# Kernel optimization log

Hardware: AMD Instinct MI355X
Metric: run time of the kernel (lower is better)

## Reference

```python
import jax, jax.numpy as jnp
import numpy as np

N_HEADS = 16

def setup_inputs() -> dict:
    key = jax.random.key(0)
    k1, k2, k3 = jax.random.split(key, 3)
    d = 1024
    x = jax.random.normal(k1, (2, 2048, d), dtype=jnp.float32)
    W_in = jax.random.normal(k2, (d, 3 * d), dtype=jnp.float32) * (d ** -0.5)
    W_out = jax.random.normal(k3, (d, d), dtype=jnp.float32) * (d ** -0.5)
    return {"x": x, "W_in": W_in, "W_out": W_out}

def reference(x, W_in, W_out):
    B, S, D = x.shape
    H = N_HEADS
    Dh = D // H
    qkv = x @ W_in                                  # [B,S,3D]
    q, k, v = jnp.split(qkv, 3, axis=-1)
    # [B,S,D] -> [B,H,S,Dh]
    q = q.reshape(B, S, H, Dh).transpose(0, 2, 1, 3)
    k = k.reshape(B, S, H, Dh).transpose(0, 2, 1, 3)
    v = v.reshape(B, S, H, Dh).transpose(0, 2, 1, 3)
    scores = jnp.einsum('bhqd,bhkd->bhqk', q, k)    # [B,H,S,S]
    causal = jnp.triu(jnp.ones((S, S), dtype=bool), k=1)
    scores = jnp.where(causal, -jnp.inf, scores)
    scores = scores / jnp.sqrt(jnp.asarray(Dh, scores.dtype))
    attn = jax.nn.softmax(scores, axis=-1)
    out = jnp.einsum('bhqk,bhkd->bhqd', attn, v)    # [B,H,S,Dh]
    out = out.transpose(0, 2, 1, 3).reshape(B, S, D)
    return out @ W_out
```

## Files before the change

kernel.cpp:

```cpp
#include <hip/hip_runtime.h>
#include <cstdint>
#include <cstddef>

typedef __bf16 bf16;
typedef bf16  bf16x4  __attribute__((ext_vector_type(4)));
typedef bf16  bf16x8  __attribute__((ext_vector_type(8)));
typedef float floatx4 __attribute__((ext_vector_type(4)));

#define BATCH 2
#define SEQ   2048
#define DIM   1024
#define NH    16
#define DH    64
#define D3    3072
#define MROWS 4096

__device__ __forceinline__ void gld16(void* lds, const void* gptr) {
  __builtin_amdgcn_global_load_lds(
      (const __attribute__((address_space(1))) unsigned int*)gptr,
      (__attribute__((address_space(3))) unsigned int*)lds, 16, 0, 0);
}

__global__ __launch_bounds__(256) void k_prep(const float4* __restrict__ x,
                                              bf16* __restrict__ xb,
                                              const float* __restrict__ Wi,
                                              bf16* __restrict__ wti,
                                              const float* __restrict__ Wo,
                                              bf16* __restrict__ wto) {
  __shared__ float tile[32][33];
  const int bid = blockIdx.x;
  if (bid < 4096) {
    int i = bid * 256 + threadIdx.x;
    float4 v = x[i];
    bf16x4 o;
    o.x = (bf16)v.x; o.y = (bf16)v.y; o.z = (bf16)v.z; o.w = (bf16)v.w;
    *(bf16x4*)(xb + (size_t)i * 4) = o;
    return;
  }
  const float* W; bf16* Wt; int N, id;
  if (bid < 7168) { W = Wi; Wt = wti; N = 3072; id = bid - 4096; }
  else            { W = Wo; Wt = wto; N = 1024; id = bid - 7168; }
  const int nb = N / 32;
  int n0 = (id % nb) * 32, k0 = (id / nb) * 32;
  int tx = threadIdx.x & 31, ty = threadIdx.x >> 5;
#pragma unroll
  for (int i = 0; i < 4; i++)
    tile[ty + i * 8][tx] = W[(size_t)(k0 + ty + i * 8) * N + n0 + tx];
  __syncthreads();
#pragma unroll
  for (int i = 0; i < 4; i++)
    Wt[(size_t)(n0 + ty + i * 8) * 1024 + k0 + tx] = (bf16)tile[tx][ty + i * 8];
}

__global__ __launch_bounds__(256, 2) void k_gemm1(const bf16* __restrict__ A,
                                                  const bf16* __restrict__ Bt,
                                                  bf16* __restrict__ qk,
                                                  bf16* __restrict__ vt) {
  constexpr int K = DIM;
  constexpr int nk = K / 64;
  __shared__ __align__(16) bf16 As[2][128 * 64];
  __shared__ __align__(16) bf16 Bs[2][192 * 64];

  const int t = threadIdx.x, l = t & 63, w = t >> 6;
  const int q = l >> 4, mm = l & 15;
  const int wm = w >> 1, wn = w & 1;

  const int xcd = blockIdx.x & 7, j = blockIdx.x >> 3;
  const int by = ((xcd >> 1) << 3) + (j >> 3);
  const int bx = ((xcd & 1) << 3) + (j & 7);
  const int m0 = by * 128, n0 = bx * 192;

  auto stA = [&](int T, int up) {
    const int bp = T & 1;
#pragma unroll
    for (int i = 0; i < 2; i++) {
      int c = t + i * 256;
      int rl = c >> 3, pos = c & 7;
      int row = ((rl >> 5) << 6) + (up << 5) + (rl & 31);
      int gs = pos ^ (row & 7);
      gld16((char*)(As[bp] + row * 64 + pos * 8),
            A + (size_t)(m0 + row) * K + T * 64 + gs * 8);
    }
  };
  auto stB = [&](int T, int up) {
    const int bp = T & 1;
#pragma unroll
    for (int i = 0; i < 3; i++) {
      int c = t + i * 256;
      int rl = c >> 3, pos = c & 7;
      int row = up * 96 + rl;
      int gs = pos ^ (row & 7);
      gld16((char*)(Bs[bp] + row * 64 + pos * 8),
            Bt + (size_t)(n0 + row) * K + T * 64 + gs * 8);
    }
  };

  floatx4 acc[4][6] = {};

  stA(0, 0); stB(0, 0); stA(0, 1); stB(0, 1);
  stA(1, 0); stB(1, 0);

  for (int T = 0; T < nk; T++) {
    const int bp = T & 1;
    if (T + 1 < nk)
      asm volatile("s_waitcnt vmcnt(5)\n\ts_barrier" ::: "memory");
    else
      asm volatile("s_waitcnt vmcnt(0)\n\ts_barrier" ::: "memory");

    const bf16* Ab = As[bp] + wm * 64 * 64;
    const bf16* Bb = Bs[bp] + wn * 96 * 64;
    bf16x8 a0[2][2], a1[2][2], b0[3][2], b1[3][2];

#pragma unroll
    for (int mt = 0; mt < 2; mt++)
#pragma unroll
      for (int kk = 0; kk < 2; kk++)
        a0[mt][kk] = *(const bf16x8*)(Ab + (size_t)(mt * 16 + mm) * 64 +
                                      ((kk * 4 + q) ^ (mm & 7)) * 8);
#pragma unroll
    for (int nt = 0; nt < 3; nt++)
#pragma unroll
      for (int kk = 0; kk < 2; kk++)
        b0[nt][kk] = *(const bf16x8*)(Bb + (size_t)(nt * 16 + mm) * 64 +
                                      ((kk * 4 + q) ^ (mm & 7)) * 8);
    if (T + 1 < nk) stA(T + 1, 1);
    asm volatile("s_barrier" ::: "memory");
    __builtin_amdgcn_s_setprio(1);
#pragma unroll
    for (int mt = 0; mt < 2; mt++)
#pragma unroll
      for (int nt = 0; nt < 3; nt++)
#pragma unroll
        for (int kk = 0; kk < 2; kk++)
          acc[mt][nt] = __builtin_amdgcn_mfma_f32_16x16x32_bf16(
              a0[mt][kk], b0[nt][kk], acc[mt][nt], 0, 0, 0);
    __builtin_amdgcn_s_setprio(0);
    asm volatile("s_barrier" ::: "memory");

#pragma unroll
    for (int nt = 0; nt < 3; nt++)
#pragma unroll
      for (int kk = 0; kk < 2; kk++)
        b1[nt][kk] = *(const bf16x8*)(Bb + (size_t)((3 + nt) * 16 + mm) * 64 +
                                      ((kk * 4 + q) ^ (mm & 7)) * 8);
    if (T + 1 < nk) stB(T + 1, 1);
    asm volatile("s_barrier" ::: "memory");
    __builtin_amdgcn_s_setprio(1);
#pragma unroll
    for (int mt = 0; mt < 2; mt++)
#pragma unroll
      for (int nt = 0; nt < 3; nt++)
#pragma unroll
        for (int kk = 0; kk < 2; kk++)
          acc[mt][3 + nt] = __builtin_amdgcn_mfma_f32_16x16x32_bf16(
              a0[mt][kk], b1[nt][kk], acc[mt][3 + nt], 0, 0, 0);
    __builtin_amdgcn_s_setprio(0);
    asm volatile("s_barrier" ::: "memory");

#pragma unroll
    for (int mt = 0; mt < 2; mt++)
#pragma unroll
      for (int kk = 0; kk < 2; kk++)
        a1[mt][kk] = *(const bf16x8*)(Ab + (size_t)(32 + mt * 16 + mm) * 64 +
                                      ((kk * 4 + q) ^ (mm & 7)) * 8);
    if (T + 2 < nk) stA(T + 2, 0);
    asm volatile("s_barrier" ::: "memory");
    __builtin_amdgcn_s_setprio(1);
#pragma unroll
    for (int mt = 0; mt < 2; mt++)
#pragma unroll
      for (int nt = 0; nt < 3; nt++)
#pragma unroll
        for (int kk = 0; kk < 2; kk++)
          acc[2 + mt][nt] = __builtin_amdgcn_mfma_f32_16x16x32_bf16(
              a1[mt][kk], b0[nt][kk], acc[2 + mt][nt], 0, 0, 0);
    __builtin_amdgcn_s_setprio(0);
    asm volatile("s_barrier" ::: "memory");

    if (T + 2 < nk) stB(T + 2, 0);
    asm volatile("s_barrier" ::: "memory");
    __builtin_amdgcn_s_setprio(1);
#pragma unroll
    for (int mt = 0; mt < 2; mt++)
#pragma unroll
      for (int nt = 0; nt < 3; nt++)
#pragma unroll
        for (int kk = 0; kk < 2; kk++)
          acc[2 + mt][3 + nt] = __builtin_amdgcn_mfma_f32_16x16x32_bf16(
              a1[mt][kk], b1[nt][kk], acc[2 + mt][3 + nt], 0, 0, 0);
    __builtin_amdgcn_s_setprio(0);
  }

#pragma unroll
  for (int mt = 0; mt < 4; mt++)
#pragma unroll
    for (int nt = 0; nt < 6; nt++) {
      int row = m0 + wm * 64 + mt * 16 + q * 4;
      int col = n0 + wn * 96 + nt * 16 + mm;
      if (col < 2048) {
#pragma unroll
        for (int r = 0; r < 4; r++)
          qk[(size_t)(row + r) * 2048 + col] = (bf16)acc[mt][nt][r];
      } else {
        int d = col - 2048;
        int hh = d >> 6, dh = d & 63;
#pragma unroll
        for (int r = 0; r < 4; r++) {
          int rr = row + r;
          int bb = rr >> 11, s = rr & 2047;
          vt[((size_t)(bb * 16 + hh) * 64 + dh) * SEQ + s] = (bf16)acc[mt][nt][r];
        }
      }
    }
}

template <typename OutT, int MODE, int BN>
__global__ __launch_bounds__(256) void k_gemm_bt(const bf16* __restrict__ A,
                                                 const bf16* __restrict__ Bt,
                                                 OutT* __restrict__ C,
                                                 bf16* __restrict__ qk,
                                                 bf16* __restrict__ vt,
                                                 int M, int N, int K) {
  constexpr int LN = 2 + BN / 64;
  __shared__ __align__(16) bf16 As[3][128 * 32];
  __shared__ __align__(16) bf16 Bs[3][BN * 32];
  const int t = threadIdx.x, l = t & 63, w = t >> 6;
  const int q = l >> 4, mm = l & 15;
  const int m0 = blockIdx.y * 128, n0 = blockIdx.x * BN;
  constexpr int MT = (BN == 128) ? 4 : 2;
  const int mo = (BN == 128) ? ((w >> 1) * 64) : (w * 32);
  const int no = (BN == 128) ? ((w & 1) * 64) : 0;
  const int sw = (mm >> 1) & 3;

  auto stage = [&](int kt) {
    const int bp = kt % 3;
#pragma unroll
    for (int i = 0; i < 2; i++) {
      int c = t + i * 256;
      int row = c >> 2, pos = c & 3;
      int gs = pos ^ ((row >> 1) & 3);
      gld16((char*)As[bp] + (size_t)c * 16, A + (size_t)(m0 + row) * K + kt * 32 + gs * 8);
    }
#pragma unroll
    for (int i = 0; i < BN / 64; i++) {
      int c = t + i * 256;
      int row = c >> 2, pos = c & 3;
      int gs = pos ^ ((row >> 1) & 3);
      gld16((char*)Bs[bp] + (size_t)c * 16, Bt + (size_t)(n0 + row) * K + kt * 32 + gs * 8);
    }
  };

  floatx4 acc[MT][4] = {};
  const int nk = K >> 5;

  stage(0);
  stage(1);

  for (int kt = 0; kt < nk; kt++) {
    if (kt + 1 < nk)
      asm volatile("s_waitcnt vmcnt(%0)\n\ts_barrier" :: "n"(LN) : "memory");
    else
      asm volatile("s_waitcnt vmcnt(0)\n\ts_barrier" ::: "memory");
    if (kt + 2 < nk) stage(kt + 2);

    const bf16* Ab = As[kt % 3];
    const bf16* Bb = Bs[kt % 3];
    bf16x8 af[MT], bfr[4];
#pragma unroll
    for (int mt = 0; mt < MT; mt++)
      af[mt] = *(const bf16x8*)(Ab + (size_t)(mo + mt * 16 + mm) * 32 + (q ^ sw) * 8);
#pragma unroll
    for (int nt = 0; nt < 4; nt++)
      bfr[nt] = *(const bf16x8*)(Bb + (size_t)(no + nt * 16 + mm) * 32 + (q ^ sw) * 8);
#pragma unroll
    for (int mt = 0; mt < MT; mt++)
#pragma unroll
      for (int nt = 0; nt < 4; nt++)
        acc[mt][nt] = __builtin_amdgcn_mfma_f32_16x16x32_bf16(af[mt], bfr[nt],
                                                              acc[mt][nt], 0, 0, 0);
  }
#pragma unroll
  for (int mt = 0; mt < MT; mt++)
#pragma unroll
    for (int nt = 0; nt < 4; nt++)
#pragma unroll
      for (int r = 0; r < 4; r++) {
        int row = m0 + mo + mt * 16 + q * 4 + r;
        int col = n0 + no + nt * 16 + mm;
        if (MODE == 0) {
          C[(size_t)row * N + col] = (OutT)acc[mt][nt][r];
        } else {
          if (col < 2048) {
            qk[(size_t)row * 2048 + col] = (bf16)acc[mt][nt][r];
          } else {
            int d = col - 2048;
            int hh = d >> 6, dh = d & 63;
            int bb = row >> 11, s = row & 2047;
            vt[((size_t)(bb * 16 + hh) * 64 + dh) * SEQ + s] = (bf16)acc[mt][nt][r];
          }
        }
      }
}

__global__ __launch_bounds__(256, 4) void k_attn(const bf16* __restrict__ qk,
                                                 const bf16* __restrict__ vt,
                                                 bf16* __restrict__ out) {
  const int bx = blockIdx.x;
  const int qt = 31 - (bx >> 5);
  const int bh = bx & 31;
  const int b = bh >> 4, h = bh & 15;
  const int t = threadIdx.x, l = t & 63, w = t >> 6;
  const int q4 = l >> 4, mm = l & 15;
  const int sw = (mm >> 1) & 3;

  __shared__ __align__(16) char lds[8192 + 16384 + 16384];
  bf16* Qs = (bf16*)lds;
  bf16* Ps = (bf16*)lds;
  bf16* Ks = (bf16*)(lds + 8192);
  bf16* Vs = (bf16*)(lds + 8192 + 16384);

  const size_t qkbase = (size_t)b * SEQ * 2048;
  const size_t vtbase = (size_t)bh * 64 * SEQ;

  auto stage = [&](int kt) {
    const int bp = kt & 1;
#pragma unroll
    for (int i = 0; i < 2; i++) {
      int row = t >> 2, pos = t & 3;
      int g = pos ^ ((row >> 1) & 3);
      gld16((char*)(Ks + bp * 4096) + ((size_t)t + i * 256) * 16,
            qk + qkbase + (size_t)(kt * 64 + row) * 2048 + 1024 + h * 64 + i * 32 + g * 8);
    }
#pragma unroll
    for (int i = 0; i < 2; i++) {
      int c = t + i * 256;
      int vr = c >> 3, vc = c & 7;
      int src = vc ^ (vr & 7);
      gld16((char*)(Vs + bp * 4096) + (size_t)c * 16,
            vt + vtbase + (size_t)vr * SEQ + kt * 64 + src * 8);
    }
  };

  {
    int row = t >> 2, col = (t & 3) * 8;
#pragma unroll
    for (int i = 0; i < 2; i++)
      gld16((char*)Qs + ((size_t)t + i * 256) * 16,
            qk + qkbase + (size_t)(qt * 64 + row) * 2048 + h * 64 + i * 32 + col);
  }
  stage(0);
  __syncthreads();
  bf16x8 qf[2];
#pragma unroll
  for (int ks = 0; ks < 2; ks++) {
    qf[ks] = *(const bf16x8*)(Qs + (size_t)(ks * 64 + w * 16 + mm) * 32 + q4 * 8);
#pragma unroll
    for (int j = 0; j < 8; j++)
      qf[ks][j] = (bf16)((float)qf[ks][j] * 0.18033688f);
  }
  __syncthreads();

  float l_i = 0.f;
  floatx4 oaccT[4] = {};
  const int qloc = w * 16 + mm;
  const float FM = 24.0f;

  bf16* Pw = Ps + (size_t)w * 640;

  for (int kt = 0; kt <= qt; kt++) {
    if (kt < qt) stage(kt + 1);
    const bf16* Kb = Ks + (kt & 1) * 4096;
    const bf16* Vb = Vs + (kt & 1) * 4096;

    floatx4 sacc[4] = {};
#pragma unroll
    for (int ks = 0; ks < 2; ks++)
#pragma unroll
      for (int ct = 0; ct < 4; ct++) {
        bf16x8 kf = *(const bf16x8*)(Kb + (size_t)(ks * 64 + ct * 16 + mm) * 32 + (q4 ^ sw) * 8);
        sacc[ct] = __builtin_amdgcn_mfma_f32_16x16x32_bf16(kf, qf[ks], sacc[ct], 0, 0, 0);
      }

    bf16x4 pk[4];
    float rsum = 0.f;
    if (kt == qt) {
#pragma unroll
      for (int ct = 0; ct < 4; ct++)
#pragma unroll
        for (int r = 0; r < 4; r++) {
          float e = (ct * 16 + q4 * 4 + r > qloc)
                        ? 0.f : __builtin_amdgcn_exp2f(sacc[ct][r] - FM);
          pk[ct][r] = (bf16)e;
          rsum += e;
        }
    } else {
#pragma unroll
      for (int ct = 0; ct < 4; ct++)
#pragma unroll
        for (int r = 0; r < 4; r++) {
          float e = __builtin_amdgcn_exp2f(sacc[ct][r] - FM);
          pk[ct][r] = (bf16)e;
          rsum += e;
        }
    }
    rsum += __shfl_xor(rsum, 16, 64);
    rsum += __shfl_xor(rsum, 32, 64);
    l_i += rsum;

#pragma unroll
    for (int ks = 0; ks < 2; ks++) {
      *(bf16x4*)(Pw + (size_t)mm * 40 + q4 * 4)      = pk[ks * 2 + 0];
      *(bf16x4*)(Pw + (size_t)mm * 40 + 16 + q4 * 4) = pk[ks * 2 + 1];
      bf16x8 pf = *(const bf16x8*)(Pw + (size_t)mm * 40 + q4 * 8);
#pragma unroll
      for (int nt = 0; nt < 4; nt++) {
        int chunk = (ks * 4 + q4) ^ (mm & 7);
        bf16x8 vf = *(const bf16x8*)(Vb + (size_t)(nt * 16 + mm) * 64 + chunk * 8);
        oaccT[nt] = __builtin_amdgcn_mfma_f32_16x16x32_bf16(vf, pf, oaccT[nt], 0, 0, 0);
      }
    }

    if (kt < qt) __syncthreads();
  }

  float inv = 1.0f / l_i;
  int qrow = qt * 64 + qloc;
  bf16* orow = out + ((size_t)b * SEQ + qrow) * DIM + h * 64;
#pragma unroll
  for (int nt = 0; nt < 4; nt++) {
    bf16x4 o4;
#pragma unroll
    for (int r = 0; r < 4; r++) o4[r] = (bf16)(oaccT[nt][r] * inv);
    *(bf16x4*)(orow + nt * 16 + q4 * 4) = o4;
  }
}

extern "C" void kernel_launch(void* const* d_in, const int* in_sizes, int n_in,
                              void* d_out, int out_size, void* d_ws, size_t ws_size,
                              hipStream_t stream) {
  const float* x     = (const float*)d_in[0];
  const float* W_in  = (const float*)d_in[1];
  const float* W_out = (const float*)d_in[2];
  float* out = (float*)d_out;

  char* ws = (char*)d_ws;
  bf16* xb   = (bf16*)(ws);
  bf16* wti  = (bf16*)(ws + 8388608);
  bf16* wto  = (bf16*)(ws + 14680064);
  bf16* qkb  = (bf16*)(ws + 16777216);
  bf16* vtb  = (bf16*)(ws + 33554432);
  bf16* attn = xb;

  k_prep<<<8192, 256, 0, stream>>>((const float4*)x, xb, W_in, wti, W_out, wto);
  k_gemm1<<<512, 256, 0, stream>>>(xb, wti, qkb, vtb);
  k_attn<<<1024, 256, 0, stream>>>(qkb, vtb, attn);
  k_gemm_bt<float, 0, 64><<<dim3(16, 32), 256, 0, stream>>>(attn, wto, out, nullptr, nullptr,
                                                            MROWS, DIM, DIM);
}
```

Before: 163.3 us.

## Double attention query tile to 128 rows per block to reuse K/V tiles

Each attention block now handles 128 query rows instead of 64: every wave holds two 16-row query groups and issues two MFMAs per K/V fragment load, which halves the K/V global-to-LDS traffic per query. The grid shrinks from 1024 to 512 blocks, LDS grows to 48KB and launch bounds drop to 2 blocks per CU to allow more registers. The cost is lower occupancy, fewer blocks for load balancing under the causal triangle, and extra masked work on the two diagonal tiles.

New measurement: 170.7 us. 4.6% more time.

```diff
diff --git a/kernel.cpp b/kernel.cpp
--- a/kernel.cpp
+++ b/kernel.cpp
@@ -302,22 +302,22 @@
       }
 }
 
-__global__ __launch_bounds__(256, 4) void k_attn(const bf16* __restrict__ qk,
+__global__ __launch_bounds__(256, 2) void k_attn(const bf16* __restrict__ qk,
                                                  const bf16* __restrict__ vt,
                                                  bf16* __restrict__ out) {
   const int bx = blockIdx.x;
-  const int qt = 31 - (bx >> 5);
+  const int qt = 15 - (bx >> 5);
   const int bh = bx & 31;
   const int b = bh >> 4, h = bh & 15;
   const int t = threadIdx.x, l = t & 63, w = t >> 6;
   const int q4 = l >> 4, mm = l & 15;
   const int sw = (mm >> 1) & 3;
 
-  __shared__ __align__(16) char lds[8192 + 16384 + 16384];
+  __shared__ __align__(16) char lds[16384 + 16384 + 16384];
   bf16* Qs = (bf16*)lds;
   bf16* Ps = (bf16*)lds;
-  bf16* Ks = (bf16*)(lds + 8192);
-  bf16* Vs = (bf16*)(lds + 8192 + 16384);
+  bf16* Ks = (bf16*)(lds + 16384);
+  bf16* Vs = (bf16*)(lds + 32768);
 
   const size_t qkbase = (size_t)b * SEQ * 2048;
   const size_t vtbase = (size_t)bh * 64 * SEQ;
@@ -342,96 +342,116 @@
   };
 
   {
-    int row = t >> 2, col = (t & 3) * 8;
-#pragma unroll
-    for (int i = 0; i < 2; i++)
-      gld16((char*)Qs + ((size_t)t + i * 256) * 16,
-            qk + qkbase + (size_t)(qt * 64 + row) * 2048 + h * 64 + i * 32 + col);
+    int row = t >> 2, c8 = (t & 3) * 8;
+#pragma unroll
+    for (int u = 0; u < 2; u++)
+#pragma unroll
+      for (int ks = 0; ks < 2; ks++)
+        gld16((char*)Qs + (size_t)ks * 8192 + u * 4096 + (size_t)t * 16,
+              qk + qkbase + (size_t)(qt * 128 + u * 64 + row) * 2048 + h * 64 + ks * 32 + c8);
   }
   stage(0);
   __syncthreads();
-  bf16x8 qf[2];
-#pragma unroll
-  for (int ks = 0; ks < 2; ks++) {
-    qf[ks] = *(const bf16x8*)(Qs + (size_t)(ks * 64 + w * 16 + mm) * 32 + q4 * 8);
-#pragma unroll
-    for (int j = 0; j < 8; j++)
-      qf[ks][j] = (bf16)((float)qf[ks][j] * 0.18033688f);
-  }
+  bf16x8 qf[2][2];
+#pragma unroll
+  for (int g = 0; g < 2; g++)
+#pragma unroll
+    for (int ks = 0; ks < 2; ks++) {
+      qf[g][ks] = *(const bf16x8*)(Qs + (size_t)ks * 4096 +
+                                   (size_t)(w * 32 + g * 16 + mm) * 32 + q4 * 8);
+#pragma unroll
+      for (int j = 0; j < 8; j++)
+        qf[g][ks][j] = (bf16)((float)qf[g][ks][j] * 0.18033688f);
+    }
   __syncthreads();
 
-  float l_i = 0.f;
-  floatx4 oaccT[4] = {};
-  const int qloc = w * 16 + mm;
+  float l_i[2] = {0.f, 0.f};
+  floatx4 oaccT[2][4] = {};
   const float FM = 24.0f;
-
-  bf16* Pw = Ps + (size_t)w * 640;
-
-  for (int kt = 0; kt <= qt; kt++) {
-    if (kt < qt) stage(kt + 1);
+  const int nkt = 2 * qt + 2;
+
+  bf16* Pw0 = Ps + (size_t)(w * 2 + 0) * 640;
+  bf16* Pw1 = Ps + (size_t)(w * 2 + 1) * 640;
+
+  for (int kt = 0; kt < nkt; kt++) {
+    if (kt + 1 < nkt) stage(kt + 1);
     const bf16* Kb = Ks + (kt & 1) * 4096;
     const bf16* Vb = Vs + (kt & 1) * 4096;
 
-    floatx4 sacc[4] = {};
+    floatx4 sacc[2][4] = {};
 #pragma unroll
     for (int ks = 0; ks < 2; ks++)
 #pragma unroll
       for (int ct = 0; ct < 4; ct++) {
         bf16x8 kf = *(const bf16x8*)(Kb + (size_t)(ks * 64 + ct * 16 + mm) * 32 + (q4 ^ sw) * 8);
-        sacc[ct] = __builtin_amdgcn_mfma_f32_16x16x32_bf16(kf, qf[ks], sacc[ct], 0, 0, 0);
+        sacc[0][ct] = __builtin_amdgcn_mfma_f32_16x16x32_bf16(kf, qf[0][ks], sacc[0][ct], 0, 0, 0);
+        sacc[1][ct] = __builtin_amdgcn_mfma_f32_16x16x32_bf16(kf, qf[1][ks], sacc[1][ct], 0, 0, 0);
       }
 
-    bf16x4 pk[4];
-    float rsum = 0.f;
-    if (kt == qt) {
+    bf16x4 pk[2][4];
+    float rs0 = 0.f, rs1 = 0.f;
+    if (kt >= 2 * qt) {
+      const int kvb = (kt - 2 * qt) * 64;
 #pragma unroll
       for (int ct = 0; ct < 4; ct++)
 #pragma unroll
         for (int r = 0; r < 4; r++) {
-          float e = (ct * 16 + q4 * 4 + r > qloc)
-                        ? 0.f : __builtin_amdgcn_exp2f(sacc[ct][r] - FM);
-          pk[ct][r] = (bf16)e;
-          rsum += e;
+          int kv = kvb + ct * 16 + q4 * 4 + r;
+          float e0 = (kv > w * 32 + mm)      ? 0.f : __builtin_amdgcn_exp2f(sacc[0][ct][r] - FM);
+          float e1 = (kv > w * 32 + 16 + mm) ? 0.f : __builtin_amdgcn_exp2f(sacc[1][ct][r] - FM);
+          pk[0][ct][r] = (bf16)e0; rs0 += e0;
+          pk[1][ct][r] = (bf16)e1; rs1 += e1;
         }
     } else {
 #pragma unroll
       for (int ct = 0; ct < 4; ct++)
 #pragma unroll
         for (int r = 0; r < 4; r++) {
-          float e = __builtin_amdgcn_exp2f(sacc[ct][r] - FM);
-          pk[ct][r] = (bf16)e;
-          rsum += e;
+          float e0 = __builtin_amdgcn_exp2f(sacc[0][ct][r] - FM);
+          float e1 = __builtin_amdgcn_exp2f(sacc[1][ct][r] - FM);
+          pk[0][ct][r] = (bf16)e0; rs0 += e0;
+          pk[1][ct][r] = (bf16)e1; rs1 += e1;
         }
     }
-    rsum += __shfl_xor(rsum, 16, 64);
-    rsum += __shfl_xor(rsum, 32, 64);
-    l_i += rsum;
+    rs0 += __shfl_xor(rs0, 16, 64);
+    rs0 += __shfl_xor(rs0, 32, 64);
+    rs1 += __shfl_xor(rs1, 16, 64);
+    rs1 += __shfl_xor(rs1, 32, 64);
+    l_i[0] += rs0;
+    l_i[1] += rs1;
 
 #pragma unroll
     for (int ks = 0; ks < 2; ks++) {
-      *(bf16x4*)(Pw + (size_t)mm * 40 + q4 * 4)      = pk[ks * 2 + 0];
-      *(bf16x4*)(Pw + (size_t)mm * 40 + 16 + q4 * 4) = pk[ks * 2 + 1];
-      bf16x8 pf = *(const bf16x8*)(Pw + (size_t)mm * 40 + q4 * 8);
+      *(bf16x4*)(Pw0 + (size_t)mm * 40 + q4 * 4)      = pk[0][ks * 2 + 0];
+      *(bf16x4*)(Pw0 + (size_t)mm * 40 + 16 + q4 * 4) = pk[0][ks * 2 + 1];
+      *(bf16x4*)(Pw1 + (size_t)mm * 40 + q4 * 4)      = pk[1][ks * 2 + 0];
+      *(bf16x4*)(Pw1 + (size_t)mm * 40 + 16 + q4 * 4) = pk[1][ks * 2 + 1];
+      bf16x8 pf0 = *(const bf16x8*)(Pw0 + (size_t)mm * 40 + q4 * 8);
+      bf16x8 pf1 = *(const bf16x8*)(Pw1 + (size_t)mm * 40 + q4 * 8);
 #pragma unroll
       for (int nt = 0; nt < 4; nt++) {
         int chunk = (ks * 4 + q4) ^ (mm & 7);
         bf16x8 vf = *(const bf16x8*)(Vb + (size_t)(nt * 16 + mm) * 64 + chunk * 8);
-        oaccT[nt] = __builtin_amdgcn_mfma_f32_16x16x32_bf16(vf, pf, oaccT[nt], 0, 0, 0);
+        oaccT[0][nt] = __builtin_amdgcn_mfma_f32_16x16x32_bf16(vf, pf0, oaccT[0][nt], 0, 0, 0);
+        oaccT[1][nt] = __builtin_amdgcn_mfma_f32_16x16x32_bf16(vf, pf1, oaccT[1][nt], 0, 0, 0);
       }
     }
 
-    if (kt < qt) __syncthreads();
-  }
-
-  float inv = 1.0f / l_i;
-  int qrow = qt * 64 + qloc;
-  bf16* orow = out + ((size_t)b * SEQ + qrow) * DIM + h * 64;
-#pragma unroll
-  for (int nt = 0; nt < 4; nt++) {
-    bf16x4 o4;
-#pragma unroll
-    for (int r = 0; r < 4; r++) o4[r] = (bf16)(oaccT[nt][r] * inv);
-    *(bf16x4*)(orow + nt * 16 + q4 * 4) = o4;
+    if (kt + 1 < nkt) __syncthreads();
+  }
+
+#pragma unroll
+  for (int g = 0; g < 2; g++) {
+    float inv = 1.0f / l_i[g];
+    int qrow = qt * 128 + w * 32 + g * 16 + mm;
+    bf16* orow = out + ((size_t)b * SEQ + qrow) * DIM + h * 64;
+#pragma unroll
+    for (int nt = 0; nt < 4; nt++) {
+      bf16x4 o4;
+#pragma unroll
+      for (int r = 0; r < 4; r++) o4[r] = (bf16)(oaccT[g][nt][r] * inv);
+      *(bf16x4*)(orow + nt * 16 + q4 * 4) = o4;
+    }
   }
 }
 
@@ -453,7 +473,7 @@
 
   k_prep<<<8192, 256, 0, stream>>>((const float4*)x, xb, W_in, wti, W_out, wto);
   k_gemm1<<<512, 256, 0, stream>>>(xb, wti, qkb, vtb);
-  k_attn<<<1024, 256, 0, stream>>>(qkb, vtb, attn);
+  k_attn<<<512, 256, 0, stream>>>(qkb, vtb, attn);
   k_gemm_bt<float, 0, 64><<<dim3(16, 32), 256, 0, stream>>>(attn, wto, out, nullptr, nullptr,
                                                             MROWS, DIM, DIM);
 }
```

## Rewrite output projection GEMM with 64-wide K tiles, split-phase pipelining and XCD-aware mapping

Applied to the files above, without the earlier changes.

Replaces the generic templated GEMM used for the output projection with a dedicated kernel. It uses 64-element K tiles with an 8-way XOR swizzle, a 2x2 warp layout, and A/B global-to-LDS prefetches split across two MFMA phases with s_setprio raised around the MFMAs. It also remaps the 1D block index so that neighbouring tiles land on the same XCD for L2 reuse. The aim is to cut the number of barrier iterations and to overlap loads with compute better. The cost is more LDS per block and extra barriers in each iteration.

Result: faster. 156.6 us (-4.1%).

```diff
diff --git a/kernel.cpp b/kernel.cpp
--- a/kernel.cpp
+++ b/kernel.cpp
@@ -214,92 +214,119 @@
     }
 }
 
-template <typename OutT, int MODE, int BN>
-__global__ __launch_bounds__(256) void k_gemm_bt(const bf16* __restrict__ A,
-                                                 const bf16* __restrict__ Bt,
-                                                 OutT* __restrict__ C,
-                                                 bf16* __restrict__ qk,
-                                                 bf16* __restrict__ vt,
-                                                 int M, int N, int K) {
-  constexpr int LN = 2 + BN / 64;
-  __shared__ __align__(16) bf16 As[3][128 * 32];
-  __shared__ __align__(16) bf16 Bs[3][BN * 32];
+__global__ __launch_bounds__(256, 2) void k_gemm2(const bf16* __restrict__ A,
+                                                  const bf16* __restrict__ Bt,
+                                                  float* __restrict__ C) {
+  constexpr int K = DIM;
+  constexpr int nk = K / 64;
+  constexpr int N = DIM;
+  __shared__ __align__(16) bf16 As[3][128 * 64];
+  __shared__ __align__(16) bf16 Bs[3][64 * 64];
+
   const int t = threadIdx.x, l = t & 63, w = t >> 6;
   const int q = l >> 4, mm = l & 15;
-  const int m0 = blockIdx.y * 128, n0 = blockIdx.x * BN;
-  constexpr int MT = (BN == 128) ? 4 : 2;
-  const int mo = (BN == 128) ? ((w >> 1) * 64) : (w * 32);
-  const int no = (BN == 128) ? ((w & 1) * 64) : 0;
-  const int sw = (mm >> 1) & 3;
-
-  auto stage = [&](int kt) {
-    const int bp = kt % 3;
+  const int wm = w >> 1, wn = w & 1;
+
+  const int xcd = blockIdx.x & 7, j = blockIdx.x >> 3;
+  const int by = ((xcd >> 1) << 3) + (j >> 3);
+  const int bx = ((xcd & 1) << 3) + (j & 7);
+  const int m0 = by * 128, n0 = bx * 64;
+
+  auto stA2 = [&](int T) {
+    const int bp = T % 3;
+#pragma unroll
+    for (int i = 0; i < 4; i++) {
+      int c = t + i * 256;
+      int row = c >> 3, pos = c & 7;
+      int gs = pos ^ (row & 7);
+      gld16((char*)(As[bp] + row * 64 + pos * 8),
+            A + (size_t)(m0 + row) * K + T * 64 + gs * 8);
+    }
+  };
+  auto stB2 = [&](int T) {
+    const int bp = T % 3;
 #pragma unroll
     for (int i = 0; i < 2; i++) {
       int c = t + i * 256;
-      int row = c >> 2, pos = c & 3;
-      int gs = pos ^ ((row >> 1) & 3);
-      gld16((char*)As[bp] + (size_t)c * 16, A + (size_t)(m0 + row) * K + kt * 32 + gs * 8);
-    }
-#pragma unroll
-    for (int i = 0; i < BN / 64; i++) {
-      int c = t + i * 256;
-      int row = c >> 2, pos = c & 3;
-      int gs = pos ^ ((row >> 1) & 3);
-      gld16((char*)Bs[bp] + (size_t)c * 16, Bt + (size_t)(n0 + row) * K + kt * 32 + gs * 8);
+      int row = c >> 3, pos = c & 7;
+      int gs = pos ^ (row & 7);
+      gld16((char*)(Bs[bp] + row * 64 + pos * 8),
+            Bt + (size_t)(n0 + row) * K + T * 64 + gs * 8);
     }
   };
 
-  floatx4 acc[MT][4] = {};
-  const int nk = K >> 5;
-
-  stage(0);
-  stage(1);
-
-  for (int kt = 0; kt < nk; kt++) {
-    if (kt + 1 < nk)
-      asm volatile("s_waitcnt vmcnt(%0)\n\ts_barrier" :: "n"(LN) : "memory");
+  floatx4 acc[4][2] = {};
+
+  stA2(0); stB2(0);
+  stA2(1); stB2(1);
+
+  for (int T = 0; T < nk; T++) {
+    const int bp = T % 3;
+    if (T + 1 < nk)
+      asm volatile("s_waitcnt vmcnt(6)\n\ts_barrier" ::: "memory");
     else
       asm volatile("s_waitcnt vmcnt(0)\n\ts_barrier" ::: "memory");
-    if (kt + 2 < nk) stage(kt + 2);
-
-    const bf16* Ab = As[kt % 3];
-    const bf16* Bb = Bs[kt % 3];
-    bf16x8 af[MT], bfr[4];
-#pragma unroll
-    for (int mt = 0; mt < MT; mt++)
-      af[mt] = *(const bf16x8*)(Ab + (size_t)(mo + mt * 16 + mm) * 32 + (q ^ sw) * 8);
-#pragma unroll
-    for (int nt = 0; nt < 4; nt++)
-      bfr[nt] = *(const bf16x8*)(Bb + (size_t)(no + nt * 16 + mm) * 32 + (q ^ sw) * 8);
-#pragma unroll
-    for (int mt = 0; mt < MT; mt++)
-#pragma unroll
-      for (int nt = 0; nt < 4; nt++)
-        acc[mt][nt] = __builtin_amdgcn_mfma_f32_16x16x32_bf16(af[mt], bfr[nt],
-                                                              acc[mt][nt], 0, 0, 0);
-  }
-#pragma unroll
-  for (int mt = 0; mt < MT; mt++)
-#pragma unroll
-    for (int nt = 0; nt < 4; nt++)
-#pragma unroll
-      for (int r = 0; r < 4; r++) {
-        int row = m0 + mo + mt * 16 + q * 4 + r;
-        int col = n0 + no + nt * 16 + mm;
-        if (MODE == 0) {
-          C[(size_t)row * N + col] = (OutT)acc[mt][nt][r];
-        } else {
-          if (col < 2048) {
-            qk[(size_t)row * 2048 + col] = (bf16)acc[mt][nt][r];
-          } else {
-            int d = col - 2048;
-            int hh = d >> 6, dh = d & 63;
-            int bb = row >> 11, s = row & 2047;
-            vt[((size_t)(bb * 16 + hh) * 64 + dh) * SEQ + s] = (bf16)acc[mt][nt][r];
-          }
-        }
-      }
+
+    const bf16* Ab = As[bp] + wm * 64 * 64;
+    const bf16* Bb = Bs[bp] + wn * 32 * 64;
+    bf16x8 af[4][2], bf[2][2];
+
+#pragma unroll
+    for (int mt = 0; mt < 2; mt++)
+#pragma unroll
+      for (int kk = 0; kk < 2; kk++)
+        af[mt][kk] = *(const bf16x8*)(Ab + (size_t)(mt * 16 + mm) * 64 +
+                                      ((kk * 4 + q) ^ (mm & 7)) * 8);
+#pragma unroll
+    for (int nt = 0; nt < 2; nt++)
+#pragma unroll
+      for (int kk = 0; kk < 2; kk++)
+        bf[nt][kk] = *(const bf16x8*)(Bb + (size_t)(nt * 16 + mm) * 64 +
+                                      ((kk * 4 + q) ^ (mm & 7)) * 8);
+    if (T + 2 < nk) stA2(T + 2);
+    asm volatile("s_barrier" ::: "memory");
+    __builtin_amdgcn_s_setprio(1);
+#pragma unroll
+    for (int mt = 0; mt < 2; mt++)
+#pragma unroll
+      for (int nt = 0; nt < 2; nt++)
+#pragma unroll
+        for (int kk = 0; kk < 2; kk++)
+          acc[mt][nt] = __builtin_amdgcn_mfma_f32_16x16x32_bf16(
+              af[mt][kk], bf[nt][kk], acc[mt][nt], 0, 0, 0);
+    __builtin_amdgcn_s_setprio(0);
+    asm volatile("s_barrier" ::: "memory");
+
+#pragma unroll
+    for (int mt = 0; mt < 2; mt++)
+#pragma unroll
+      for (int kk = 0; kk < 2; kk++)
+        af[2 + mt][kk] = *(const bf16x8*)(Ab + (size_t)(32 + mt * 16 + mm) * 64 +
+                                          ((kk * 4 + q) ^ (mm & 7)) * 8);
+    if (T + 2 < nk) stB2(T + 2);
+    asm volatile("s_barrier" ::: "memory");
+    __builtin_amdgcn_s_setprio(1);
+#pragma unroll
+    for (int mt = 0; mt < 2; mt++)
+#pragma unroll
+      for (int nt = 0; nt < 2; nt++)
+#pragma unroll
+        for (int kk = 0; kk < 2; kk++)
+          acc[2 + mt][nt] = __builtin_amdgcn_mfma_f32_16x16x32_bf16(
+              af[2 + mt][kk], bf[nt][kk], acc[2 + mt][nt], 0, 0, 0);
+    __builtin_amdgcn_s_setprio(0);
+  }
+
+#pragma unroll
+  for (int mt = 0; mt < 4; mt++)
+#pragma unroll
+    for (int nt = 0; nt < 2; nt++) {
+      int row = m0 + wm * 64 + mt * 16 + q * 4;
+      int col = n0 + wn * 32 + nt * 16 + mm;
+#pragma unroll
+      for (int r = 0; r < 4; r++)
+        C[(size_t)(row + r) * N + col] = acc[mt][nt][r];
+    }
 }
 
 __global__ __launch_bounds__(256, 4) void k_attn(const bf16* __restrict__ qk,
@@ -454,6 +481,5 @@
   k_prep<<<8192, 256, 0, stream>>>((const float4*)x, xb, W_in, wti, W_out, wto);
   k_gemm1<<<512, 256, 0, stream>>>(xb, wti, qkb, vtb);
   k_attn<<<1024, 256, 0, stream>>>(qkb, vtb, attn);
-  k_gemm_bt<float, 0, 64><<<dim3(16, 32), 256, 0, stream>>>(attn, wto, out, nullptr, nullptr,
-                                                            MROWS, DIM, DIM);
-}
+  k_gemm2<<<512, 256, 0, stream>>>(attn, wto, out);
+}
```
